# Kernel tuning notes

Hardware: AMD Instinct MI355X
Metric: run time of the kernel (lower is better)

Reference implementation:

```python
import jax, jax.numpy as jnp
import numpy as np

NUM_HEADS = 8


def _mha(x, w_in, b_in, w_out, b_out, nh=NUM_HEADS):
    # x: [B, L, H]; torch nn.MultiheadAttention (batch_first) self-attention
    B, L, H = x.shape
    dh = H // nh
    qkv = x @ w_in.T + b_in                      # [B, L, 3H]
    q, k, v = jnp.split(qkv, 3, axis=-1)
    def heads(t):
        return t.reshape(B, L, nh, dh).transpose(0, 2, 1, 3)  # [B, nh, L, dh]
    q, k, v = heads(q), heads(k), heads(v)
    scale = 1.0 / np.sqrt(dh)
    scores = jnp.einsum('bhqd,bhkd->bhqk', q * scale, k)      # [B, nh, L, L]
    attn = jax.nn.softmax(scores, axis=-1)
    out = jnp.einsum('bhqk,bhkd->bhqd', attn, v)               # [B, nh, L, dh]
    out = out.transpose(0, 2, 1, 3).reshape(B, L, H)
    return out @ w_out.T + b_out


def setup_inputs() -> dict:
    key = jax.random.key(0)
    ks = jax.random.split(key, 10)
    S, M, B, H = 64, 4, 128, 1024
    std = 0.02
    inp = {
        'hidden_states_combined': jax.random.normal(ks[0], (S, M, B, 1, H), jnp.float32),
        'mf_in_w': jax.random.normal(ks[1], (3 * H, H), jnp.float32) * std,
        'mf_in_b': jnp.zeros((3 * H,), jnp.float32),
        'mf_out_w': jax.random.normal(ks[2], (H, H), jnp.float32) * std,
        'mf_out_b': jnp.zeros((H,), jnp.float32),
        'sf_in_w': jax.random.normal(ks[3], (3 * H, H), jnp.float32) * std,
        'sf_in_b': jnp.zeros((3 * H,), jnp.float32),
        'sf_out_w': jax.random.normal(ks[4], (H, H), jnp.float32) * std,
        'sf_out_b': jnp.zeros((H,), jnp.float32),
        'pos_enc': jax.random.normal(ks[5], (1, S, H), jnp.float32) * std,
    }
    return inp


def reference(hidden_states_combined, mf_in_w, mf_in_b, mf_out_w, mf_out_b,
              sf_in_w, sf_in_b, sf_out_w, sf_out_b, pos_enc):
    S, M, B, _, H = hidden_states_combined.shape
    # [S, M, B, 1, H] -> [S, B, M, H] -> batch all steps together: [S*B, M, H]
    x = hidden_states_combined[:, :, :, 0, :].transpose(0, 2, 1, 3).reshape(S * B, M, H)
    fused = _mha(x, mf_in_w, mf_in_b, mf_out_w, mf_out_b)        # [S*B, M, H]
    fused = fused.mean(axis=1).reshape(S, B, H)                  # mean over models
    seq = fused.transpose(1, 0, 2) + pos_enc[:, :S, :]            # [B, S, H]
    enhanced = _mha(seq, sf_in_w, sf_in_b, sf_out_w, sf_out_b)   # [B, S, H]
    return enhanced.transpose(1, 0, 2)[:, :, None, :]             # [S, B, 1, H]
```

## Files before the change

### kernel.cpp

```cpp
#include <hip/hip_runtime.h>

typedef unsigned short u16;
typedef __attribute__((ext_vector_type(8))) short bf16x8;
typedef __attribute__((ext_vector_type(4))) float f32x4;

__device__ __forceinline__ u16 f2bf(float f) {
  unsigned u = __float_as_uint(f);
  u += 0x7FFFu + ((u >> 16) & 1u);
  return (u16)(u >> 16);
}
__device__ __forceinline__ float bf2f(u16 h) {
  return __uint_as_float(((unsigned)h) << 16);
}

#define GLOAD16(g, l) __builtin_amdgcn_global_load_lds( \
    (const __attribute__((address_space(1))) void*)(g), \
    (__attribute__((address_space(3))) void*)(l), 16, 0, 0)

__global__ __launch_bounds__(256) void cvtw4_kernel(const float* __restrict__ s0, u16* __restrict__ d0,
                                                    const float* __restrict__ s1, u16* __restrict__ d1,
                                                    const float* __restrict__ s2, u16* __restrict__ d2,
                                                    const float* __restrict__ s3, u16* __restrict__ d3) {
  int i = blockIdx.x * 256 + threadIdx.x;
  const float* s; u16* d; int off;
  if (i < 786432)       { s = s0; d = d0; off = i; }
  else if (i < 1048576) { s = s1; d = d1; off = i - 786432; }
  else if (i < 1835008) { s = s2; d = d2; off = i - 1048576; }
  else                  { s = s3; d = d3; off = i - 1835008; }
  float4 f = ((const float4*)s)[off];
  ushort4 u;
  u.x = f2bf(f.x); u.y = f2bf(f.y); u.z = f2bf(f.z); u.w = f2bf(f.w);
  ((ushort4*)d)[off] = u;
}

__global__ __launch_bounds__(256) void xcvt_kernel(const float* __restrict__ hidden,
                                                   u16* __restrict__ xb, int s0) {
  int idx = blockIdx.x * 256 + threadIdx.x;
  int h4 = idx & 255;
  int lrow = idx >> 8;
  int m = lrow & 3;
  int b = (lrow >> 2) & 127;
  int sl = lrow >> 9;
  int s = s0 + sl;
  const float4 f = *(const float4*)(hidden + (((size_t)(s * 4 + m) * 128 + b) * 1024) + h4 * 4);
  ushort4 u;
  u.x = f2bf(f.x); u.y = f2bf(f.y); u.z = f2bf(f.z); u.w = f2bf(f.w);
  *(ushort4*)(xb + (size_t)lrow * 1024 + h4 * 4) = u;
}

template <int KK>
__global__ __launch_bounds__(512, 2) void gemm8p(const u16* __restrict__ A,
                                                 const u16* __restrict__ Bw,
                                                 const float* __restrict__ bias,
                                                 u16* __restrict__ C, int N) {
  __shared__ u16 Sh[65536];
  const int t = threadIdx.x, w = t >> 6, l = t & 63;
  const int lr = l & 15, lg = l >> 4;
  const int wm = w >> 2, wn = w & 3;

  const int gx = gridDim.x;
  const int nb = gx * gridDim.y;
  const int id = blockIdx.y * gx + blockIdx.x;
  const int id2 = (id & 7) * (nb >> 3) + (id >> 3);
  const int rowBase = (id2 / gx) * 256, colBase = (id2 % gx) * 256;

  const int sslot8 = ((t & 3) ^ ((t >> 3) & 3)) * 8;
  const u16* Ag = A + (size_t)(rowBase + (t >> 2)) * KK + sslot8;
  const u16* Bg = Bw + (size_t)(colBase + (t >> 2)) * KK + sslot8;
  const size_t K128 = (size_t)128 * KK;
  const int ldsW = w * 512;

  const int fslot8 = (lg ^ ((lr >> 1) & 3)) * 8;
  const int aRowOff = (wm * 128 + lr) * 32 + fslot8;
  const int bRowOff = (wn * 64 + lr) * 32 + fslot8;

  f32x4 acc[8][4];
#pragma unroll
  for (int i = 0; i < 8; i++)
#pragma unroll
    for (int j = 0; j < 4; j++) acc[i][j] = (f32x4){0.f, 0.f, 0.f, 0.f};
  bf16x8 af[2][4], bfr[2][4];

#define STGA(tt, KH, DB) { \
    const u16* g_ = Ag + (size_t)(tt) * 64 + (KH) * 32; \
    GLOAD16(g_, Sh + ((DB) * 2 + (KH)) * 8192 + ldsW); \
    GLOAD16(g_ + K128, Sh + ((DB) * 2 + (KH)) * 8192 + 4096 + ldsW); }
#define STGB(tt, KH, DB) { \
    const u16* g_ = Bg + (size_t)(tt) * 64 + (KH) * 32; \
    GLOAD16(g_, Sh + 32768 + ((DB) * 2 + (KH)) * 8192 + ldsW); \
    GLOAD16(g_ + K128, Sh + 32768 + ((DB) * 2 + (KH)) * 8192 + 4096 + ldsW); }

#define RA(DD, KH, MG, BUF) { \
    const u16* sa_ = Sh + ((DD) * 2 + (KH)) * 8192 + aRowOff; \
    _Pragma("unroll") \
    for (int mi = 0; mi < 4; mi++) af[BUF][mi] = *(const bf16x8*)(sa_ + ((MG) * 4 + mi) * 512); }
#define RB(DD, KH, BUF) { \
    const u16* sb_ = Sh + 32768 + ((DD) * 2 + (KH)) * 8192 + bRowOff; \
    _Pragma("unroll") \
    for (int n = 0; n < 4; n++) bfr[BUF][n] = *(const bf16x8*)(sb_ + n * 512); }

#define LG(NN) asm volatile("s_waitcnt lgkmcnt(" #NN ")" ::: "memory"); \
               __builtin_amdgcn_sched_barrier(0)
#define WTC(NN) asm volatile("s_waitcnt vmcnt(" #NN ")" ::: "memory")
#define BAR asm volatile("s_barrier" ::: "memory")

#define MM(MG, AB, BB) { \
    __builtin_amdgcn_s_setprio(1); \
    _Pragma("unroll") \
    for (int mi = 0; mi < 4; mi++) { \
      _Pragma("unroll") \
      for (int n = 0; n < 4; n++) \
        acc[(MG) * 4 + mi][n] = __builtin_amdgcn_mfma_f32_16x16x32_bf16( \
            af[AB][mi], bfr[BB][n], acc[(MG) * 4 + mi][n], 0, 0, 0); \
    } \
    __builtin_amdgcn_s_setprio(0); }

  STGA(0, 0, 0); STGB(0, 0, 0);
  STGA(0, 1, 0); STGB(0, 1, 0);
  STGA(1, 0, 1); STGB(1, 0, 1);
  WTC(8);
  BAR;
  RA(0, 0, 0, 0); RB(0, 0, 0);

  const int NIT = KK / 128;
  int t0 = 0;
  for (int it = 0; it < NIT - 1; ++it, t0 += 2) {
    STGA(t0 + 1, 1, 1); RA(0, 0, 1, 1);              LG(4); MM(0, 0, 0); WTC(6); BAR;
    STGB(t0 + 1, 1, 1); RA(0, 1, 0, 0); RB(0, 1, 1); LG(8); MM(1, 1, 0);         BAR;
    STGA(t0 + 2, 0, 0); RA(0, 1, 1, 1);              LG(4); MM(0, 0, 1); WTC(6); BAR;
    STGB(t0 + 2, 0, 0); RA(1, 0, 0, 0); RB(1, 0, 0); LG(8); MM(1, 1, 1);         BAR;
    STGA(t0 + 2, 1, 0); RA(1, 0, 1, 1);              LG(4); MM(0, 0, 0); WTC(6); BAR;
    STGB(t0 + 2, 1, 0); RA(1, 1, 0, 0); RB(1, 1, 1); LG(8); MM(1, 1, 0);         BAR;
    STGA(t0 + 3, 0, 1); RA(1, 1, 1, 1);              LG(4); MM(0, 0, 1); WTC(6); BAR;
    STGB(t0 + 3, 0, 1); RA(0, 0, 0, 0); RB(0, 0, 0); LG(8); MM(1, 1, 1);         BAR;
  }
  STGA(t0 + 1, 1, 1); RA(0, 0, 1, 1);              LG(4); MM(0, 0, 0); WTC(6); BAR;
  STGB(t0 + 1, 1, 1); RA(0, 1, 0, 0); RB(0, 1, 1); LG(8); MM(1, 1, 0);         BAR;
  RA(0, 1, 1, 1);                                  LG(4); MM(0, 0, 1); WTC(4); BAR;
  RA(1, 0, 0, 0); RB(1, 0, 0);                     LG(8); MM(1, 1, 1);         BAR;
  RA(1, 0, 1, 1);                                  LG(4); MM(0, 0, 0); WTC(0); BAR;
  RA(1, 1, 0, 0); RB(1, 1, 1);                     LG(8); MM(1, 1, 0);         BAR;
  RA(1, 1, 1, 1);                                  LG(4); MM(0, 0, 1);         BAR;
                                                   LG(0); MM(1, 1, 1);
#undef MM
#undef BAR
#undef WTC
#undef LG
#undef RB
#undef RA
#undef STGB
#undef STGA

  const int orow0 = rowBase + wm * 128 + lg * 4;
  const int ocol0 = colBase + wn * 64 + lr;
#pragma unroll
  for (int m = 0; m < 8; m++) {
#pragma unroll
    for (int n = 0; n < 4; n++) {
      const int col = ocol0 + n * 16;
      const float bv = bias[col];
#pragma unroll
      for (int r = 0; r < 4; r++) {
        const int row = orow0 + m * 16 + r;
        C[(size_t)row * N + col] = f2bf(acc[m][n][r] + bv);
      }
    }
  }
}

template <int MODE>
__global__ __launch_bounds__(256, 2) void gemm_fp(const u16* __restrict__ A,
                                                  const u16* __restrict__ Bw,
                                                  const float* __restrict__ bias,
                                                  void* __restrict__ Cout,
                                                  int N, int K,
                                                  const float* __restrict__ posenc) {
  __shared__ u16 SA[3][8192];
  __shared__ u16 SB[3][4096];
  const int t = threadIdx.x, w = t >> 6, l = t & 63;
  const int lr = l & 15, lg = l >> 4;
  const int wm = w >> 1, wn = w & 1;

  const int gx = gridDim.x;
  const int nb = gx * gridDim.y;
  const int id = blockIdx.y * gx + blockIdx.x;
  const int id2 = (id & 7) * (nb >> 3) + (id >> 3);
  const int rowBase = (id2 / gx) * 256, colBase = (id2 % gx) * 128;

  const int srow = l >> 2;
  const int ssl = ((l & 3) ^ (srow & 3)) * 8;
  const u16* Ag = A + (size_t)(rowBase + w * 16 + srow) * K + ssl;
  const u16* Bg = Bw + (size_t)(colBase + w * 16 + srow) * K + ssl;
  u16* const lA = &SA[0][0] + w * 512;
  u16* const lB = &SB[0][0] + w * 512;

  const int fsw = (lg ^ (lr & 3)) * 8;
  const int aoff = (wm * 128 + lr) * 32 + fsw;
  const int boff = (wn * 64 + lr) * 32 + fsw;

  f32x4 acc[8][4];
#pragma unroll
  for (int i = 0; i < 8; i++)
#pragma unroll
    for (int j = 0; j < 4; j++) acc[i][j] = (f32x4){0.f, 0.f, 0.f, 0.f};

#define STG_P0(tt, bb) do { \
    const size_t ko_ = (size_t)(tt) * 32; \
    GLOAD16(Ag + ko_,                    lA + (bb) * 8192); \
    GLOAD16(Ag + ko_ + (size_t)64 * K,   lA + (bb) * 8192 + 2048); \
    GLOAD16(Ag + ko_ + (size_t)128 * K,  lA + (bb) * 8192 + 4096); \
  } while (0)
#define STG_P1(tt, bb) do { \
    const size_t ko_ = (size_t)(tt) * 32; \
    GLOAD16(Ag + ko_ + (size_t)192 * K,  lA + (bb) * 8192 + 6144); \
    GLOAD16(Bg + ko_,                    lB + (bb) * 4096); \
    GLOAD16(Bg + ko_ + (size_t)64 * K,   lB + (bb) * 4096 + 2048); \
  } while (0)
#define FBAR asm volatile("s_barrier" ::: "memory")

  const int nt = K >> 5;
  STG_P0(0, 0); STG_P1(0, 0);
  STG_P0(1, 1); STG_P1(1, 1);
  asm volatile("s_waitcnt vmcnt(6)" ::: "memory");
  FBAR;

  int bcur = 0;
  for (int tt = 0; tt < nt; ++tt) {
    const u16* pa = &SA[bcur][0];
    const u16* pb = &SB[bcur][0];
    const int bnext = (bcur + 2 > 2) ? bcur - 1 : bcur + 2;
    bf16x8 af[4], bfr[4];

#pragma unroll
    for (int m = 0; m < 4; m++) af[m] = *(const bf16x8*)(pa + aoff + m * 512);
#pragma unroll
    for (int n = 0; n < 4; n++) bfr[n] = *(const bf16x8*)(pb + boff + n * 512);
    if (tt + 2 < nt) STG_P0(tt + 2, bnext);
    FBAR;
    asm volatile("s_waitcnt lgkmcnt(0)" ::: "memory");
    __builtin_amdgcn_sched_barrier(0);
    __builtin_amdgcn_s_setprio(1);
#pragma unroll
    for (int m = 0; m < 4; m++)
#pragma unroll
      for (int n = 0; n < 4; n++)
        acc[m][n] = __builtin_amdgcn_mfma_f32_16x16x32_bf16(af[m], bfr[n], acc[m][n], 0, 0, 0);
    __builtin_amdgcn_s_setprio(0);
    FBAR;

#pragma unroll
    for (int m = 0; m < 4; m++) af[m] = *(const bf16x8*)(pa + aoff + (m + 4) * 512);
    if (tt + 2 < nt) STG_P1(tt + 2, bnext);
    FBAR;
    asm volatile("s_waitcnt lgkmcnt(0)" ::: "memory");
    __builtin_amdgcn_sched_barrier(0);
    __builtin_amdgcn_s_setprio(1);
#pragma unroll
    for (int m = 0; m < 4; m++)
#pragma unroll
      for (int n = 0; n < 4; n++)
        acc[m + 4][n] = __builtin_amdgcn_mfma_f32_16x16x32_bf16(af[m], bfr[n], acc[m + 4][n], 0, 0, 0);
    __builtin_amdgcn_s_setprio(0);
    if (tt + 2 < nt) {
      asm volatile("s_waitcnt vmcnt(6)" ::: "memory");
    } else if (tt + 1 < nt) {
      asm volatile("s_waitcnt vmcnt(0)" ::: "memory");
    }
    FBAR;
    bcur = (bcur + 1 > 2) ? 0 : bcur + 1;
  }
#undef FBAR
#undef STG_P0
#undef STG_P1

  const int orow0 = rowBase + wm * 128 + lg * 4;
  const int ocol0 = colBase + wn * 64 + lr;
#pragma unroll
  for (int m = 0; m < 8; m++) {
#pragma unroll
    for (int n = 0; n < 4; n++) {
      const int col = ocol0 + n * 16;
      const float bv = bias[col];
#pragma unroll
      for (int r = 0; r < 4; r++) {
        const int row = orow0 + m * 16 + r;
        float v = acc[m][n][r] + bv;
        if (MODE == 1) {
          int s = row >> 7, b = row & 127;
          v += posenc[s * 1024 + col];
          ((u16*)Cout)[((size_t)(b * 64 + s)) * 1024 + col] = f2bf(v);
        } else {
          int s = row & 63, b = row >> 6;
          ((float*)Cout)[((size_t)(s * 128 + b)) * 1024 + col] = v;
        }
      }
    }
  }
}

__global__ __launch_bounds__(256) void attn1_kernel(const u16* __restrict__ qkv,
                                                    u16* __restrict__ am, int seqBase) {
  const int w = threadIdx.x >> 6, l = threadIdx.x & 63;
  const int pair = blockIdx.x * 4 + w;
  const int seq = pair >> 3, head = pair & 7;
  const int d0 = l * 2;
  const u16* base = qkv + (size_t)(seq * 4) * 3072 + head * 128 + d0;
  const float scale = 0.08838834764831845f;
  float q[4][2], k[4][2], v[4][2];
#pragma unroll
  for (int m = 0; m < 4; m++) {
    ushort2 uq = *(const ushort2*)(base + (size_t)m * 3072);
    ushort2 uk = *(const ushort2*)(base + (size_t)m * 3072 + 1024);
    ushort2 uv = *(const ushort2*)(base + (size_t)m * 3072 + 2048);
    q[m][0] = bf2f(uq.x) * scale; q[m][1] = bf2f(uq.y) * scale;
    k[m][0] = bf2f(uk.x);         k[m][1] = bf2f(uk.y);
    v[m][0] = bf2f(uv.x);         v[m][1] = bf2f(uv.y);
  }
  float sc[4][4];
#pragma unroll
  for (int i = 0; i < 4; i++)
#pragma unroll
    for (int j = 0; j < 4; j++)
      sc[i][j] = q[i][0] * k[j][0] + q[i][1] * k[j][1];
#pragma unroll
  for (int off = 32; off >= 1; off >>= 1)
#pragma unroll
    for (int i = 0; i < 4; i++)
#pragma unroll
      for (int j = 0; j < 4; j++)
        sc[i][j] += __shfl_xor(sc[i][j], off, 64);
  float pbar[4] = {0.f, 0.f, 0.f, 0.f};
#pragma unroll
  for (int i = 0; i < 4; i++) {
    float mx = fmaxf(fmaxf(sc[i][0], sc[i][1]), fmaxf(sc[i][2], sc[i][3]));
    float e0 = __expf(sc[i][0] - mx), e1 = __expf(sc[i][1] - mx);
    float e2 = __expf(sc[i][2] - mx), e3 = __expf(sc[i][3] - mx);
    float inv = 0.25f / (e0 + e1 + e2 + e3);
    pbar[0] += e0 * inv; pbar[1] += e1 * inv; pbar[2] += e2 * inv; pbar[3] += e3 * inv;
  }
  float o0 = pbar[0] * v[0][0] + pbar[1] * v[1][0] + pbar[2] * v[2][0] + pbar[3] * v[3][0];
  float o1 = pbar[0] * v[0][1] + pbar[1] * v[1][1] + pbar[2] * v[2][1] + pbar[3] * v[3][1];
  ushort2 ou; ou.x = f2bf(o0); ou.y = f2bf(o1);
  *(ushort2*)(am + (size_t)(seqBase + seq) * 1024 + head * 128 + d0) = ou;
}

__global__ __launch_bounds__(256) void attn2_kernel(const u16* __restrict__ qkv2,
                                                    u16* __restrict__ aout) {
  __shared__ u16 Qs[64 * 128];
  __shared__ u16 Ks[64 * 128];
  __shared__ u16 Vt[128 * 72];
  __shared__ u16 Ps[64 * 72];
  const int t = threadIdx.x, w = t >> 6, l = t & 63;
  const int lr = l & 15, lg = l >> 4;
  const int b = blockIdx.x >> 3, head = blockIdx.x & 7;
  const u16* qb = qkv2 + (size_t)(b * 64) * 3072 + head * 128;

#pragma unroll
  for (int c = 0; c < 4; c++) {
    int flat = c * 256 + t;
    int row = flat >> 4, sp = flat & 15;
    int sg = (sp ^ (row & 7)) * 8;
    GLOAD16(qb + (size_t)row * 3072 + sg, Qs + (c * 256 + w * 64) * 8);
    GLOAD16(qb + 1024 + (size_t)row * 3072 + sg, Ks + (c * 256 + w * 64) * 8);
  }
  const int dd = (t & 63) * 2, kb = t >> 6;
#pragma unroll
  for (int c = 0; c < 16; c++) {
    int k = c * 4 + kb;
    ushort2 vv = *(const ushort2*)(qb + 2048 + (size_t)k * 3072 + dd);
    Vt[(size_t)dd * 72 + k] = vv.x;
    Vt[(size_t)(dd + 1) * 72 + k] = vv.y;
  }
  __syncthreads();

  f32x4 sc[4];
#pragma unroll
  for (int cb = 0; cb < 4; cb++) sc[cb] = (f32x4){0.f, 0.f, 0.f, 0.f};
#pragma unroll
  for (int ks = 0; ks < 4; ks++) {
    bf16x8 aq = *(const bf16x8*)(Qs + (w * 16 + lr) * 128 + ((ks * 4 + lg) ^ (lr & 7)) * 8);
#pragma unroll
    for (int cb = 0; cb < 4; cb++) {
      bf16x8 bk = *(const bf16x8*)(Ks + (cb * 16 + lr) * 128 + ((ks * 4 + lg) ^ (lr & 7)) * 8);
      sc[cb] = __builtin_amdgcn_mfma_f32_16x16x32_bf16(aq, bk, sc[cb], 0, 0, 0);
    }
  }

  const float scale = 0.08838834764831845f;
#pragma unroll
  for (int r = 0; r < 4; r++) {
#pragma unroll
    for (int cb = 0; cb < 4; cb++) sc[cb][r] *= scale;
    float mx = fmaxf(fmaxf(sc[0][r], sc[1][r]), fmaxf(sc[2][r], sc[3][r]));
#pragma unroll
    for (int off = 1; off < 16; off <<= 1) mx = fmaxf(mx, __shfl_xor(mx, off, 64));
    float sum = 0.f;
#pragma unroll
    for (int cb = 0; cb < 4; cb++) {
      float e = __expf(sc[cb][r] - mx);
      sum += e;
      sc[cb][r] = e;
    }
#pragma unroll
    for (int off = 1; off < 16; off <<= 1) sum += __shfl_xor(sum, off, 64);
    float inv = 1.f / sum;
    int prow = w * 16 + lg * 4 + r;
#pragma unroll
    for (int cb = 0; cb < 4; cb++)
      Ps[(size_t)prow * 72 + cb * 16 + lr] = f2bf(sc[cb][r] * inv);
  }

  f32x4 o[8];
#pragma unroll
  for (int cb = 0; cb < 8; cb++) o[cb] = (f32x4){0.f, 0.f, 0.f, 0.f};
#pragma unroll
  for (int ks = 0; ks < 2; ks++) {
    bf16x8 ap = *(const bf16x8*)(Ps + (w * 16 + lr) * 72 + ks * 32 + lg * 8);
#pragma unroll
    for (int cb = 0; cb < 8; cb++) {
      bf16x8 bv = *(const bf16x8*)(Vt + (cb * 16 + lr) * 72 + ks * 32 + lg * 8);
      o[cb] = __builtin_amdgcn_mfma_f32_16x16x32_bf16(ap, bv, o[cb], 0, 0, 0);
    }
  }
#pragma unroll
  for (int cb = 0; cb < 8; cb++) {
#pragma unroll
    for (int r = 0; r < 4; r++) {
      int srow = w * 16 + lg * 4 + r;
      int d = cb * 16 + lr;
      aout[(size_t)(b * 64 + srow) * 1024 + head * 128 + d] = f2bf(o[cb][r]);
    }
  }
}

extern "C" void kernel_launch(void* const* d_in, const int* in_sizes, int n_in,
                              void* d_out, int out_size, void* d_ws, size_t ws_size,
                              hipStream_t stream) {
  const float* hidden   = (const float*)d_in[0];
  const float* mf_in_w  = (const float*)d_in[1];
  const float* mf_in_b  = (const float*)d_in[2];
  const float* mf_out_w = (const float*)d_in[3];
  const float* mf_out_b = (const float*)d_in[4];
  const float* sf_in_w  = (const float*)d_in[5];
  const float* sf_in_b  = (const float*)d_in[6];
  const float* sf_out_w = (const float*)d_in[7];
  const float* sf_out_b = (const float*)d_in[8];
  const float* pos_enc  = (const float*)d_in[9];

  char* ws = (char*)d_ws;
  u16* w_mf_in  = (u16*)(ws);
  u16* w_mf_out = (u16*)(ws + 6291456);
  u16* w_sf_in  = (u16*)(ws + 8388608);
  u16* w_sf_out = (u16*)(ws + 14680064);

  cvtw4_kernel<<<8192, 256, 0, stream>>>(mf_in_w, w_mf_in, mf_out_w, w_mf_out,
                                         sf_in_w, w_sf_in, sf_out_w, w_sf_out);

  if (ws_size >= 201326592ull) {
    u16* xchunk   = (u16*)(ws + 16777216);
    u16* qkvbuf   = (u16*)(ws + 50331648);
    u16* attnmean = (u16*)(ws + 150994944);
    u16* seqbuf   = (u16*)(ws + 167772160);
    u16* a2out    = (u16*)(ws + 184549376);

    for (int c = 0; c < 2; ++c) {
      xcvt_kernel<<<16384, 256, 0, stream>>>(hidden, xchunk, c * 32);
      gemm8p<1024><<<dim3(12, 64), 512, 0, stream>>>(xchunk, w_mf_in, mf_in_b, qkvbuf, 3072);
      attn1_kernel<<<8192, 256, 0, stream>>>(qkvbuf, attnmean, c * 4096);
    }

    gemm_fp<1><<<dim3(8, 32), 256, 0, stream>>>(attnmean, w_mf_out, mf_out_b, seqbuf,
                                                1024, 1024, pos_enc);
    gemm8p<1024><<<dim3(12, 32), 512, 0, stream>>>(seqbuf, w_sf_in, sf_in_b, qkvbuf, 3072);
    attn2_kernel<<<1024, 256, 0, stream>>>(qkvbuf, a2out);
    gemm_fp<2><<<dim3(8, 32), 256, 0, stream>>>(a2out, w_sf_out, sf_out_b, d_out,
                                                1024, 1024, nullptr);
  } else {
    u16* xchunk   = (u16*)(ws + 16777216);
    u16* qkvbuf   = (u16*)(ws + 33554432);
    u16* attnmean = (u16*)(ws + 83886080);
    u16* seqbuf   = (u16*)(ws + 100663296);
    u16* a2out    = (u16*)(ws + 117440512);

    for (int c = 0; c < 4; ++c) {
      xcvt_kernel<<<8192, 256, 0, stream>>>(hidden, xchunk, c * 16);
      gemm8p<1024><<<dim3(12, 32), 512, 0, stream>>>(xchunk, w_mf_in, mf_in_b, qkvbuf, 3072);
      attn1_kernel<<<4096, 256, 0, stream>>>(qkvbuf, attnmean, c * 2048);
    }

    gemm_fp<1><<<dim3(8, 32), 256, 0, stream>>>(attnmean, w_mf_out, mf_out_b, seqbuf,
                                                1024, 1024, pos_enc);
    gemm8p<1024><<<dim3(12, 32), 512, 0, stream>>>(seqbuf, w_sf_in, sf_in_b, qkvbuf, 3072);
    attn2_kernel<<<1024, 256, 0, stream>>>(qkvbuf, a2out);
    gemm_fp<2><<<dim3(8, 32), 256, 0, stream>>>(a2out, w_sf_out, sf_out_b, d_out,
                                                1024, 1024, nullptr);
  }
}
```

Before: 467.4 us.

## Add 4-wave 256x256 GEMM with 128x128 per-wave tiles for QKV projection

Adds a new bf16 MFMA GEMM kernel that uses 256 threads (4 waves) per 256x256 block. Each wave computes a 128x128 sub-tile with 64 accumulators, double-buffered global-to-LDS loads, and interleaved half-tile fragment reads and MFMAs. It replaces the 8-wave gemm8p in the first-stage input projection. The aim is more register-level reuse per wave and fewer LDS reads per MFMA, at the cost of very high register pressure and one block per CU.

```diff
diff --git a/kernel.cpp b/kernel.cpp
--- a/kernel.cpp
+++ b/kernel.cpp
@@ -46,6 +46,141 @@
   ushort4 u;
   u.x = f2bf(f.x); u.y = f2bf(f.y); u.z = f2bf(f.z); u.w = f2bf(f.w);
   *(ushort4*)(xb + (size_t)lrow * 1024 + h4 * 4) = u;
+}
+
+template <int KK>
+__global__ __launch_bounds__(256, 1) void gemm_bw(const u16* __restrict__ A,
+                                                  const u16* __restrict__ Bw,
+                                                  const float* __restrict__ bias,
+                                                  u16* __restrict__ C, int N) {
+  __shared__ u16 Sh[65536];
+  const int t = threadIdx.x, w = t >> 6, l = t & 63;
+  const int lr = l & 15, lg = l >> 4;
+  const int wm = w >> 1, wn = w & 1;
+
+  const int gx = gridDim.x;
+  const int nb = gx * gridDim.y;
+  const int id = blockIdx.y * gx + blockIdx.x;
+  const int id2 = (id & 7) * (nb >> 3) + (id >> 3);
+  const int rowBase = (id2 / gx) * 256, colBase = (id2 % gx) * 256;
+
+  const int sslot8 = ((t & 3) ^ ((t >> 3) & 3)) * 8;
+  const u16* Ag = A + (size_t)(rowBase + (t >> 2)) * KK + sslot8;
+  const u16* Bg = Bw + (size_t)(colBase + (t >> 2)) * KK + sslot8;
+  const size_t K64 = (size_t)64 * KK;
+  const int ldsW = w * 512;
+
+  const int fslot8 = (lg ^ ((lr >> 1) & 3)) * 8;
+  const int aRowOff = (wm * 128 + lr) * 32 + fslot8;
+  const int bRowOff = (wn * 128 + lr) * 32 + fslot8;
+
+  f32x4 acc[8][8];
+#pragma unroll
+  for (int i = 0; i < 8; i++)
+#pragma unroll
+    for (int j = 0; j < 8; j++) acc[i][j] = (f32x4){0.f, 0.f, 0.f, 0.f};
+  bf16x8 af[2][8], bfr[2][8];
+
+#define STGA(tt, KH, DB) { \
+    const u16* g_ = Ag + (size_t)(tt) * 64 + (KH) * 32; \
+    u16* d_ = Sh + ((DB) * 2 + (KH)) * 8192 + ldsW; \
+    GLOAD16(g_, d_); GLOAD16(g_ + K64, d_ + 2048); \
+    GLOAD16(g_ + 2 * K64, d_ + 4096); GLOAD16(g_ + 3 * K64, d_ + 6144); }
+#define STGB(tt, KH, DB) { \
+    const u16* g_ = Bg + (size_t)(tt) * 64 + (KH) * 32; \
+    u16* d_ = Sh + 32768 + ((DB) * 2 + (KH)) * 8192 + ldsW; \
+    GLOAD16(g_, d_); GLOAD16(g_ + K64, d_ + 2048); \
+    GLOAD16(g_ + 2 * K64, d_ + 4096); GLOAD16(g_ + 3 * K64, d_ + 6144); }
+
+#define RAx(DD, KH, BUF) { \
+    const u16* sa_ = Sh + ((DD) * 2 + (KH)) * 8192 + aRowOff; \
+    _Pragma("unroll") \
+    for (int mi = 0; mi < 8; mi++) af[BUF][mi] = *(const bf16x8*)(sa_ + mi * 512); }
+#define RBx(DD, KH, BUF) { \
+    const u16* sb_ = Sh + 32768 + ((DD) * 2 + (KH)) * 8192 + bRowOff; \
+    _Pragma("unroll") \
+    for (int n = 0; n < 8; n++) bfr[BUF][n] = *(const bf16x8*)(sb_ + n * 512); }
+
+#define LG(NN) asm volatile("s_waitcnt lgkmcnt(" #NN ")" ::: "memory"); \
+               __builtin_amdgcn_sched_barrier(0)
+#define WTC(NN) asm volatile("s_waitcnt vmcnt(" #NN ")" ::: "memory")
+#define BAR asm volatile("s_barrier" ::: "memory")
+
+#define MMH(MLO, BUF) { \
+    __builtin_amdgcn_s_setprio(1); \
+    _Pragma("unroll") \
+    for (int mi = 0; mi < 4; mi++) { \
+      _Pragma("unroll") \
+      for (int n = 0; n < 8; n++) \
+        acc[(MLO) + mi][n] = __builtin_amdgcn_mfma_f32_16x16x32_bf16( \
+            af[BUF][(MLO) + mi], bfr[BUF][n], acc[(MLO) + mi][n], 0, 0, 0); \
+    } \
+    __builtin_amdgcn_s_setprio(0); }
+
+  STGA(0, 0, 0); STGB(0, 0, 0);
+  STGA(0, 1, 0); STGB(0, 1, 0);
+  STGA(1, 0, 1); STGB(1, 0, 1);
+  WTC(8);
+  BAR;
+  RAx(0, 0, 0); RBx(0, 0, 0);
+
+  const int nt = KK / 64;
+  for (int tt = 0; tt < nt; ++tt) {
+    const int DD = tt & 1;
+    RAx(DD, 1, 1);
+    if (tt + 1 < nt) STGA(tt + 1, 1, DD ^ 1);
+    LG(8);
+    MMH(0, 0);
+    RBx(DD, 1, 1);
+    if (tt + 1 < nt) STGB(tt + 1, 1, DD ^ 1);
+    LG(8);
+    MMH(4, 0);
+    if (tt + 1 < nt) { WTC(8); }
+    BAR;
+    if (tt + 1 < nt) {
+      RAx(DD ^ 1, 0, 0);
+      if (tt + 2 < nt) STGA(tt + 2, 0, DD);
+      LG(8);
+    } else {
+      LG(0);
+    }
+    MMH(0, 1);
+    if (tt + 1 < nt) {
+      RBx(DD ^ 1, 0, 0);
+      if (tt + 2 < nt) STGB(tt + 2, 0, DD);
+      LG(8);
+    } else {
+      LG(0);
+    }
+    MMH(4, 1);
+    if (tt + 2 < nt) { WTC(8); }
+    else if (tt + 1 < nt) { WTC(0); }
+    BAR;
+  }
+#undef MMH
+#undef BAR
+#undef WTC
+#undef LG
+#undef RBx
+#undef RAx
+#undef STGB
+#undef STGA
+
+  const int orow0 = rowBase + wm * 128 + lg * 4;
+  const int ocol0 = colBase + wn * 128 + lr;
+#pragma unroll
+  for (int m = 0; m < 8; m++) {
+#pragma unroll
+    for (int n = 0; n < 8; n++) {
+      const int col = ocol0 + n * 16;
+      const float bv = bias[col];
+#pragma unroll
+      for (int r = 0; r < 4; r++) {
+        const int row = orow0 + m * 16 + r;
+        C[(size_t)row * N + col] = f2bf(acc[m][n][r] + bv);
+      }
+    }
+  }
 }
 
 template <int KK>
@@ -465,7 +600,7 @@
 
     for (int c = 0; c < 2; ++c) {
       xcvt_kernel<<<16384, 256, 0, stream>>>(hidden, xchunk, c * 32);
-      gemm8p<1024><<<dim3(12, 64), 512, 0, stream>>>(xchunk, w_mf_in, mf_in_b, qkvbuf, 3072);
+      gemm_bw<1024><<<dim3(12, 64), 256, 0, stream>>>(xchunk, w_mf_in, mf_in_b, qkvbuf, 3072);
       attn1_kernel<<<8192, 256, 0, stream>>>(qkvbuf, attnmean, c * 4096);
     }
 
@@ -484,7 +619,7 @@
 
     for (int c = 0; c < 4; ++c) {
       xcvt_kernel<<<8192, 256, 0, stream>>>(hidden, xchunk, c * 16);
-      gemm8p<1024><<<dim3(12, 32), 512, 0, stream>>>(xchunk, w_mf_in, mf_in_b, qkvbuf, 3072);
+      gemm_bw<1024><<<dim3(12, 32), 256, 0, stream>>>(xchunk, w_mf_in, mf_in_b, qkvbuf, 3072);
       attn1_kernel<<<4096, 256, 0, stream>>>(qkvbuf, attnmean, c * 2048);
     }
 
```

New measurement: 475.3 us. Within noise of the previous version (+1.7%).

## Restructure GEMM main loop into four-phase pipeline with full-tile MFMA blocks

Applied to the files above, without the earlier changes.

Replaces the eight-phase software pipeline in the bf16 MFMA GEMM with a four-phase loop per 64-wide K tile. Each phase loads all eight A fragments and four B fragments, then issues 32 MFMAs. Because fewer phases run per K step, the loop needs fewer barriers and waitcnt points. In exchange it holds twice as many A fragment registers, which risks register pressure at two blocks per CU, and it hides LDS read latency less finely.

```diff
diff --git a/kernel.cpp b/kernel.cpp
--- a/kernel.cpp
+++ b/kernel.cpp
@@ -49,7 +49,7 @@
 }
 
 template <int KK>
-__global__ __launch_bounds__(512, 2) void gemm8p(const u16* __restrict__ A,
+__global__ __launch_bounds__(512, 2) void gemm4p(const u16* __restrict__ A,
                                                  const u16* __restrict__ Bw,
                                                  const float* __restrict__ bias,
                                                  u16* __restrict__ C, int N) {
@@ -79,7 +79,7 @@
   for (int i = 0; i < 8; i++)
 #pragma unroll
     for (int j = 0; j < 4; j++) acc[i][j] = (f32x4){0.f, 0.f, 0.f, 0.f};
-  bf16x8 af[2][4], bfr[2][4];
+  bf16x8 af[2][8], bfr[2][4];
 
 #define STGA(tt, KH, DB) { \
     const u16* g_ = Ag + (size_t)(tt) * 64 + (KH) * 32; \
@@ -90,11 +90,11 @@
     GLOAD16(g_, Sh + 32768 + ((DB) * 2 + (KH)) * 8192 + ldsW); \
     GLOAD16(g_ + K128, Sh + 32768 + ((DB) * 2 + (KH)) * 8192 + 4096 + ldsW); }
 
-#define RA(DD, KH, MG, BUF) { \
+#define RA8(DD, KH, BUF) { \
     const u16* sa_ = Sh + ((DD) * 2 + (KH)) * 8192 + aRowOff; \
     _Pragma("unroll") \
-    for (int mi = 0; mi < 4; mi++) af[BUF][mi] = *(const bf16x8*)(sa_ + ((MG) * 4 + mi) * 512); }
-#define RB(DD, KH, BUF) { \
+    for (int mi = 0; mi < 8; mi++) af[BUF][mi] = *(const bf16x8*)(sa_ + mi * 512); }
+#define RB4(DD, KH, BUF) { \
     const u16* sb_ = Sh + 32768 + ((DD) * 2 + (KH)) * 8192 + bRowOff; \
     _Pragma("unroll") \
     for (int n = 0; n < 4; n++) bfr[BUF][n] = *(const bf16x8*)(sb_ + n * 512); }
@@ -104,50 +104,51 @@
 #define WTC(NN) asm volatile("s_waitcnt vmcnt(" #NN ")" ::: "memory")
 #define BAR asm volatile("s_barrier" ::: "memory")
 
-#define MM(MG, AB, BB) { \
+#define MM32(BUF) { \
     __builtin_amdgcn_s_setprio(1); \
     _Pragma("unroll") \
-    for (int mi = 0; mi < 4; mi++) { \
+    for (int mi = 0; mi < 8; mi++) { \
       _Pragma("unroll") \
       for (int n = 0; n < 4; n++) \
-        acc[(MG) * 4 + mi][n] = __builtin_amdgcn_mfma_f32_16x16x32_bf16( \
-            af[AB][mi], bfr[BB][n], acc[(MG) * 4 + mi][n], 0, 0, 0); \
+        acc[mi][n] = __builtin_amdgcn_mfma_f32_16x16x32_bf16( \
+            af[BUF][mi], bfr[BUF][n], acc[mi][n], 0, 0, 0); \
     } \
     __builtin_amdgcn_s_setprio(0); }
 
   STGA(0, 0, 0); STGB(0, 0, 0);
   STGA(0, 1, 0); STGB(0, 1, 0);
   STGA(1, 0, 1); STGB(1, 0, 1);
-  WTC(8);
+  WTC(4);
   BAR;
-  RA(0, 0, 0, 0); RB(0, 0, 0);
-
-  const int NIT = KK / 128;
-  int t0 = 0;
-  for (int it = 0; it < NIT - 1; ++it, t0 += 2) {
-    STGA(t0 + 1, 1, 1); RA(0, 0, 1, 1);              LG(4); MM(0, 0, 0); WTC(6); BAR;
-    STGB(t0 + 1, 1, 1); RA(0, 1, 0, 0); RB(0, 1, 1); LG(8); MM(1, 1, 0);         BAR;
-    STGA(t0 + 2, 0, 0); RA(0, 1, 1, 1);              LG(4); MM(0, 0, 1); WTC(6); BAR;
-    STGB(t0 + 2, 0, 0); RA(1, 0, 0, 0); RB(1, 0, 0); LG(8); MM(1, 1, 1);         BAR;
-    STGA(t0 + 2, 1, 0); RA(1, 0, 1, 1);              LG(4); MM(0, 0, 0); WTC(6); BAR;
-    STGB(t0 + 2, 1, 0); RA(1, 1, 0, 0); RB(1, 1, 1); LG(8); MM(1, 1, 0);         BAR;
-    STGA(t0 + 3, 0, 1); RA(1, 1, 1, 1);              LG(4); MM(0, 0, 1); WTC(6); BAR;
-    STGB(t0 + 3, 0, 1); RA(0, 0, 0, 0); RB(0, 0, 0); LG(8); MM(1, 1, 1);         BAR;
-  }
-  STGA(t0 + 1, 1, 1); RA(0, 0, 1, 1);              LG(4); MM(0, 0, 0); WTC(6); BAR;
-  STGB(t0 + 1, 1, 1); RA(0, 1, 0, 0); RB(0, 1, 1); LG(8); MM(1, 1, 0);         BAR;
-  RA(0, 1, 1, 1);                                  LG(4); MM(0, 0, 1); WTC(4); BAR;
-  RA(1, 0, 0, 0); RB(1, 0, 0);                     LG(8); MM(1, 1, 1);         BAR;
-  RA(1, 0, 1, 1);                                  LG(4); MM(0, 0, 0); WTC(0); BAR;
-  RA(1, 1, 0, 0); RB(1, 1, 1);                     LG(8); MM(1, 1, 0);         BAR;
-  RA(1, 1, 1, 1);                                  LG(4); MM(0, 0, 1);         BAR;
-                                                   LG(0); MM(1, 1, 1);
-#undef MM
+  RA8(0, 0, 0); RB4(0, 0, 0);
+
+  const int nt = KK / 64;
+  for (int tt = 0; tt < nt; ++tt) {
+    const int dd = tt & 1;
+    RA8(dd, 1, 1); RB4(dd, 1, 1);
+    if (tt + 1 < nt) { STGA(tt + 1, 1, dd ^ 1); STGB(tt + 1, 1, dd ^ 1); }
+    LG(12);
+    MM32(0);
+    if (tt + 1 < nt) { WTC(4); }
+    BAR;
+    if (tt + 1 < nt) {
+      RA8(dd ^ 1, 0, 0); RB4(dd ^ 1, 0, 0);
+      if (tt + 2 < nt) { STGA(tt + 2, 0, dd); STGB(tt + 2, 0, dd); }
+      LG(12);
+    } else {
+      LG(0);
+    }
+    MM32(1);
+    if (tt + 2 < nt) { WTC(4); }
+    else if (tt + 1 < nt) { WTC(0); }
+    BAR;
+  }
+#undef MM32
 #undef BAR
 #undef WTC
 #undef LG
-#undef RB
-#undef RA
+#undef RB4
+#undef RA8
 #undef STGB
 #undef STGA
 
@@ -465,13 +466,13 @@
 
     for (int c = 0; c < 2; ++c) {
       xcvt_kernel<<<16384, 256, 0, stream>>>(hidden, xchunk, c * 32);
-      gemm8p<1024><<<dim3(12, 64), 512, 0, stream>>>(xchunk, w_mf_in, mf_in_b, qkvbuf, 3072);
+      gemm4p<1024><<<dim3(12, 64), 512, 0, stream>>>(xchunk, w_mf_in, mf_in_b, qkvbuf, 3072);
       attn1_kernel<<<8192, 256, 0, stream>>>(qkvbuf, attnmean, c * 4096);
     }
 
     gemm_fp<1><<<dim3(8, 32), 256, 0, stream>>>(attnmean, w_mf_out, mf_out_b, seqbuf,
                                                 1024, 1024, pos_enc);
-    gemm8p<1024><<<dim3(12, 32), 512, 0, stream>>>(seqbuf, w_sf_in, sf_in_b, qkvbuf, 3072);
+    gemm4p<1024><<<dim3(12, 32), 512, 0, stream>>>(seqbuf, w_sf_in, sf_in_b, qkvbuf, 3072);
     attn2_kernel<<<1024, 256, 0, stream>>>(qkvbuf, a2out);
     gemm_fp<2><<<dim3(8, 32), 256, 0, stream>>>(a2out, w_sf_out, sf_out_b, d_out,
                                                 1024, 1024, nullptr);
@@ -484,13 +485,13 @@
 
     for (int c = 0; c < 4; ++c) {
       xcvt_kernel<<<8192, 256, 0, stream>>>(hidden, xchunk, c * 16);
-      gemm8p<1024><<<dim3(12, 32), 512, 0, stream>>>(xchunk, w_mf_in, mf_in_b, qkvbuf, 3072);
+      gemm4p<1024><<<dim3(12, 32), 512, 0, stream>>>(xchunk, w_mf_in, mf_in_b, qkvbuf, 3072);
       attn1_kernel<<<4096, 256, 0, stream>>>(qkvbuf, attnmean, c * 2048);
     }
 
     gemm_fp<1><<<dim3(8, 32), 256, 0, stream>>>(attnmean, w_mf_out, mf_out_b, seqbuf,
                                                 1024, 1024, pos_enc);
-    gemm8p<1024><<<dim3(12, 32), 512, 0, stream>>>(seqbuf, w_sf_in, sf_in_b, qkvbuf, 3072);
+    gemm4p<1024><<<dim3(12, 32), 512, 0, stream>>>(seqbuf, w_sf_in, sf_in_b, qkvbuf, 3072);
     attn2_kernel<<<1024, 256, 0, stream>>>(qkvbuf, a2out);
     gemm_fp<2><<<dim3(8, 32), 256, 0, stream>>>(a2out, w_sf_out, sf_out_b, d_out,
                                                 1024, 1024, nullptr);
```

After: 467.7 us. Within noise of the previous version (+0.1%).
